# Kernel tuning notes

Measured on AMD Instinct MI355X. Metric: run time of the kernel, lower is better.

The kernel has to match this reference:

```python
import jax, jax.numpy as jnp
import numpy as np

B, N, HID, NH = 8, 1024, 1024, 16
HD = HID // NH  # head_dim = 64
MLP = 4 * HID
EPS = 1e-6


def _xavier(key, fan_in, fan_out):
    lim = np.sqrt(6.0 / (fan_in + fan_out))
    return jax.random.uniform(key, (fan_in, fan_out), jnp.float32, -lim, lim)


def setup_inputs() -> dict:
    key = jax.random.key(0)
    ks = jax.random.split(key, 10)
    return {
        "x": jax.random.normal(ks[0], (B, N, HID), jnp.float32),
        "c": jax.random.normal(ks[1], (B, HID), jnp.float32),
        "w_ada": _xavier(ks[2], HID, 6 * HID), "b_ada": jnp.zeros((6 * HID,), jnp.float32),
        "wq": _xavier(ks[3], HID, HID), "bq": jnp.zeros((HID,), jnp.float32),
        "wk": _xavier(ks[4], HID, HID), "bk": jnp.zeros((HID,), jnp.float32),
        "wv": _xavier(ks[5], HID, HID), "bv": jnp.zeros((HID,), jnp.float32),
        "wo": _xavier(ks[6], HID, HID), "bo": jnp.zeros((HID,), jnp.float32),
        "w1": _xavier(ks[7], HID, MLP), "b1": jnp.zeros((MLP,), jnp.float32),
        "w2": _xavier(ks[8], MLP, HID), "b2": jnp.zeros((HID,), jnp.float32),
    }


def _ln(t):
    # LayerNorm, elementwise_affine=False, eps=1e-6
    mu = jnp.mean(t, axis=-1, keepdims=True)
    var = jnp.mean(jnp.square(t - mu), axis=-1, keepdims=True)
    return (t - mu) * jax.lax.rsqrt(var + EPS)


def _modulate(t, shift, scale):
    return t * (1.0 + scale[:, None, :]) + shift[:, None, :]


def reference(x, c, w_ada, b_ada, wq, bq, wk, bk, wv, bv, wo, bo, w1, b1, w2, b2):
    cmod = jax.nn.silu(c) @ w_ada + b_ada  # [B, 6*HID]
    sh_msa, sc_msa, g_msa, sh_mlp, sc_mlp, g_mlp = jnp.split(cmod, 6, axis=-1)

    xm = _modulate(_ln(x), sh_msa, sc_msa)  # [B, N, HID]
    q = (xm @ wq + bq).reshape(B, N, NH, HD)
    k = (xm @ wk + bk).reshape(B, N, NH, HD)
    v = (xm @ wv + bv).reshape(B, N, NH, HD)

    # NOTE: original scales by 1/head_dim (not 1/sqrt(head_dim)), fp32 softmax
    scores = jnp.einsum('bihd,bjhd->bhij', q, k) / HD
    attn = jax.nn.softmax(scores.astype(jnp.float32), axis=-1)
    out = jnp.einsum('bhij,bjhd->bihd', attn, v).astype(v.dtype)
    out = out.reshape(B, N, HID) @ wo + bo

    x = x + g_msa[:, None, :] * out

    xm2 = _modulate(_ln(x), sh_mlp, sc_mlp)
    h = jax.nn.gelu(xm2 @ w1 + b1, approximate=False)  # nn.GELU default = exact
    mlp_out = h @ w2 + b2
    return x + g_mlp[:, None, :] * mlp_out
```

## Files before the change

### kernel.cpp

```cpp
#include <hip/hip_runtime.h>
#include <hip/hip_bf16.h>
#include <cstdint>


typedef __bf16 bf16;
typedef __attribute__((ext_vector_type(8))) __bf16 bf16x8;
typedef __attribute__((ext_vector_type(4))) __bf16 bf16x4;
typedef __attribute__((ext_vector_type(4))) float f32x4;

#define SEQ   1024
#define NHID  1024
#define NHEAD 16
#define HDIM  64
#define CMS   6144

#define GLD16(gp, lp)                                                  \
  __builtin_amdgcn_global_load_lds(                                    \
      (const __attribute__((address_space(1))) void*)(gp),             \
      (__attribute__((address_space(3))) void*)(lp), 16, 0, 0)

template <int N> __device__ __forceinline__ void vmwait() {
  if constexpr (N == 0)      asm volatile("s_waitcnt vmcnt(0)" ::: "memory");
  else if constexpr (N == 5) asm volatile("s_waitcnt vmcnt(5)" ::: "memory");
  else if constexpr (N == 6) asm volatile("s_waitcnt vmcnt(6)" ::: "memory");
}

#define BAR()                                                          \
  { asm volatile("" ::: "memory");                                     \
    __builtin_amdgcn_s_barrier();                                      \
    asm volatile("" ::: "memory"); }

struct TP4 { const float* s[4]; bf16* d[4]; };

__global__ __launch_bounds__(256) void transpose_conv4(TP4 p)
{
  __shared__ float tile[32][33];
  const float* __restrict__ src = p.s[blockIdx.z];
  bf16* __restrict__ dst = p.d[blockIdx.z];
  int n0 = blockIdx.x * 32, k0 = blockIdx.y * 32;
  int tx = threadIdx.x & 31, ty = threadIdx.x >> 5;
#pragma unroll
  for (int i = 0; i < 32; i += 8)
    tile[ty + i][tx] = src[(size_t)(k0 + ty + i) * 1024 + n0 + tx];
  __syncthreads();
#pragma unroll
  for (int i = 0; i < 32; i += 8)
    dst[(size_t)(n0 + ty + i) * 1024 + k0 + tx] = (bf16)tile[tx][ty + i];
}

__global__ __launch_bounds__(256) void transpose_conv(
    const float* __restrict__ src, bf16* __restrict__ dst, int K, int N)
{
  __shared__ float tile[32][33];
  int n0 = blockIdx.x * 32, k0 = blockIdx.y * 32;
  int tx = threadIdx.x & 31, ty = threadIdx.x >> 5;
#pragma unroll
  for (int i = 0; i < 32; i += 8)
    tile[ty + i][tx] = src[(size_t)(k0 + ty + i) * N + n0 + tx];
  __syncthreads();
#pragma unroll
  for (int i = 0; i < 32; i += 8)
    dst[(size_t)(n0 + ty + i) * K + k0 + tx] = (bf16)tile[tx][ty + i];
}

__global__ __launch_bounds__(256) void ada_kernel(
    const float* __restrict__ c, const float* __restrict__ w_ada,
    const float* __restrict__ b_ada, float* __restrict__ cmod)
{
  __shared__ float cs[1024];
  int b = blockIdx.y;
  int col = blockIdx.x * 256 + threadIdx.x;
  for (int i = threadIdx.x; i < 1024; i += 256) {
    float cv = c[b * 1024 + i];
    cs[i] = cv / (1.0f + __expf(-cv));
  }
  __syncthreads();
  float acc = b_ada[col];
#pragma unroll 8
  for (int kk = 0; kk < 1024; kk++)
    acc += cs[kk] * w_ada[(size_t)kk * CMS + col];
  cmod[b * CMS + col] = acc;
}

__global__ __launch_bounds__(256) void ln_mod(
    const float* __restrict__ x, const float* __restrict__ cmod,
    bf16* __restrict__ out, int sh_off, int sc_off)
{
  int row = blockIdx.x, b = row >> 10, tid = threadIdx.x;
  const float4* xr = (const float4*)(x + (size_t)row * NHID);
  float4 v = xr[tid];
  float s  = v.x + v.y + v.z + v.w;
  float s2 = v.x * v.x + v.y * v.y + v.z * v.z + v.w * v.w;
#pragma unroll
  for (int off = 32; off; off >>= 1) {
    s  += __shfl_xor(s, off);
    s2 += __shfl_xor(s2, off);
  }
  __shared__ float red1[4], red2[4];
  int wave = tid >> 6, lane = tid & 63;
  if (lane == 0) { red1[wave] = s; red2[wave] = s2; }
  __syncthreads();
  float S  = red1[0] + red1[1] + red1[2] + red1[3];
  float S2 = red2[0] + red2[1] + red2[2] + red2[3];
  float mean = S * (1.0f / NHID);
  float var  = S2 * (1.0f / NHID) - mean * mean;
  float rs   = rsqrtf(var + 1e-6f);
  const float4* shp = (const float4*)(cmod + b * CMS + sh_off);
  const float4* scp = (const float4*)(cmod + b * CMS + sc_off);
  float4 sh4 = shp[tid], sc4 = scp[tid];
  bf16x4 o4;
  o4[0] = (bf16)((v.x - mean) * rs * (1.0f + sc4.x) + sh4.x);
  o4[1] = (bf16)((v.y - mean) * rs * (1.0f + sc4.y) + sh4.y);
  o4[2] = (bf16)((v.z - mean) * rs * (1.0f + sc4.z) + sh4.z);
  o4[3] = (bf16)((v.w - mean) * rs * (1.0f + sc4.w) + sh4.w);
  *(bf16x4*)(out + (size_t)row * NHID + tid * 4) = o4;
}

template <int EPI, int BN>
__global__ __launch_bounds__(512, 2) void gemm8(
    const bf16* __restrict__ A, const bf16* __restrict__ Bt,
    const float* __restrict__ bias, const float* __restrict__ bias2,
    const float* __restrict__ bias3,
    bf16* __restrict__ outb, bf16* __restrict__ outb2,
    bf16* __restrict__ outb3, float* __restrict__ outf,
    const float* __restrict__ cmod, int gate_off,
    const float* __restrict__ resid,
    int N, int K)
{
  constexpr int BNH   = BN / 2;
  constexpr int LB    = BNH / 64;
  constexpr int MF    = BN / 64;
  constexpr int WC    = BN / 64;
  constexpr int WRS   = MF * 16;
  constexpr int VMN   = (LB == 2) ? 6 : 5;
  constexpr int BOFF  = 65536;
  constexpr int BBUF  = BNH * 256;
  constexpr int BHALF = BNH * 128;

  extern __shared__ __align__(16) char smem[];

  const int tid  = threadIdx.x;
  const int bm = blockIdx.y * 256, bn = blockIdx.x * BN;
  const int wave = tid >> 6, lane = tid & 63;
  const int wr = wave / WC, wc = wave % WC;
  const int l16 = lane & 15, q4 = lane >> 4;

  const int rq = tid >> 3;
  const int ch = ((tid & 7) ^ (rq & 7)) * 8;
  const int wbase = (tid & 448) * 16;

  const int aRowB = (wr * WRS + l16) * 128;
  const int bRowB = (wc * 32 + l16) * 128;
  const int slotB = (q4 ^ (l16 & 7)) * 16;

  f32x4 acc[2][2][MF][2];
#pragma unroll
  for (int a0 = 0; a0 < 2; a0++)
#pragma unroll
    for (int a1 = 0; a1 < 2; a1++)
#pragma unroll
      for (int a2 = 0; a2 < MF; a2++)
#pragma unroll
        for (int a3 = 0; a3 < 2; a3++) acc[a0][a1][a2][a3] = (f32x4)0.0f;

  auto stA = [&](int buf, int half, int T) {
    const bf16* g = A + (size_t)(bm + half * 128 + rq) * K + T * 64 + ch;
    char* l = smem + buf * 32768 + half * 16384 + wbase;
    GLD16(g, l);
    GLD16(g + (size_t)64 * K, l + 8192);
  };
  auto stB = [&](int buf, int half, int T) {
    const bf16* g = Bt + (size_t)(bn + half * BNH + rq) * K + T * 64 + ch;
    char* l = smem + BOFF + buf * BBUF + half * BHALF + wbase;
    GLD16(g, l);
    if constexpr (LB == 2) { GLD16(g + (size_t)64 * K, l + 8192); }
  };

#define RDA(BUF, QM, FR)                                                   \
  { const char* ab_ = smem + (BUF) * 32768 + (QM) * 16384 + aRowB;         \
    _Pragma("unroll")                                                      \
    for (int ks = 0; ks < 2; ks++) {                                       \
      const int sb_ = slotB ^ (ks * 64);                                   \
      _Pragma("unroll")                                                    \
      for (int mf = 0; mf < MF; mf++)                                      \
        FR[ks][mf] = *(const bf16x8*)(ab_ + mf * 2048 + sb_);              \
    } }

#define RDB(BUF, QN, FR)                                                   \
  { const char* bb_ = smem + BOFF + (BUF) * BBUF + (QN) * BHALF + bRowB;   \
    _Pragma("unroll")                                                      \
    for (int ks = 0; ks < 2; ks++) {                                       \
      const int sb_ = slotB ^ (ks * 64);                                   \
      _Pragma("unroll")                                                    \
      for (int nf = 0; nf < 2; nf++)                                       \
        FR[ks][nf] = *(const bf16x8*)(bb_ + nf * 2048 + sb_);              \
    } }

#define MM(QM, QN, AF, BF)                                                 \
  { __builtin_amdgcn_s_setprio(1);                                         \
    _Pragma("unroll")                                                      \
    for (int mf = 0; mf < MF; mf++)                                        \
      _Pragma("unroll")                                                    \
      for (int nf = 0; nf < 2; nf++) {                                     \
        acc[QM][QN][mf][nf] = __builtin_amdgcn_mfma_f32_16x16x32_bf16(     \
            AF[0][mf], BF[0][nf], acc[QM][QN][mf][nf], 0, 0, 0);           \
        acc[QM][QN][mf][nf] = __builtin_amdgcn_mfma_f32_16x16x32_bf16(     \
            AF[1][mf], BF[1][nf], acc[QM][QN][mf][nf], 0, 0, 0);           \
      }                                                                    \
    __builtin_amdgcn_s_setprio(0); }

  const int NT = K >> 6, NI = NT >> 1;

  bf16x8 afr[2][MF], bfr0[2][2], bfr1[2][2];

  stA(0, 0, 0); stB(0, 0, 0); stB(0, 1, 0); stA(0, 1, 0);
  stA(1, 0, 1); stB(1, 0, 1); stB(1, 1, 1); stA(1, 1, 1);

  for (int i = 0; i < NI; ++i) {
    const int t = 2 * i;
    const int u2 = (t + 2 < NT) ? t + 2 : 0;
    const int u3 = (t + 3 < NT) ? t + 3 : 0;
    vmwait<VMN>(); BAR();
    RDA(0, 0, afr); RDB(0, 0, bfr0);
    MM(0, 0, afr, bfr0);
    BAR();
    RDB(0, 1, bfr1);
    stA(0, 0, u2); stB(0, 0, u2);
    MM(0, 1, afr, bfr1);
    BAR();
    RDA(0, 1, afr);
    stB(0, 1, u2);
    MM(1, 1, afr, bfr1);
    BAR();
    stA(0, 1, u2);
    MM(1, 0, afr, bfr0);
    vmwait<VMN>(); BAR();
    RDA(1, 0, afr); RDB(1, 0, bfr0);
    MM(0, 0, afr, bfr0);
    BAR();
    RDB(1, 1, bfr1);
    stA(1, 0, u3); stB(1, 0, u3);
    MM(0, 1, afr, bfr1);
    BAR();
    RDA(1, 1, afr);
    stB(1, 1, u3);
    MM(1, 1, afr, bfr1);
    BAR();
    stA(1, 1, u3);
    MM(1, 0, afr, bfr0);
  }
  vmwait<0>();
#undef RDA
#undef RDB
#undef MM

  const int colBase = bn + wc * 32 + l16;
  const int rowBase = bm + wr * WRS + q4 * 4;
#pragma unroll
  for (int qm = 0; qm < 2; qm++)
#pragma unroll
  for (int qn = 0; qn < 2; qn++)
#pragma unroll
  for (int mf = 0; mf < MF; mf++)
#pragma unroll
  for (int nf = 0; nf < 2; nf++) {
    const int col  = colBase + qn * BNH + nf * 16;
    const int row0 = rowBase + qm * 128 + mf * 16;
    f32x4 v = acc[qm][qn][mf][nf];
    if constexpr (EPI == 5) {
      const int sel = bn >> 10;
      const float* bp = (sel == 0) ? bias : (sel == 1) ? bias2 : bias3;
      const int colq = col & 1023;
      const float bcol = bp[colq];
      if (sel == 2) {
        bf16x4 o4;
#pragma unroll
        for (int r = 0; r < 4; r++) o4[r] = (bf16)(v[r] + bcol);
        const int bidx = row0 >> 10;
        *(bf16x4*)(outb3 + ((size_t)bidx * NHID + colq) * SEQ +
                   (row0 & 1023)) = o4;
      } else {
        bf16* qk = (sel == 0) ? outb : outb2;
#pragma unroll
        for (int r = 0; r < 4; r++)
          qk[(size_t)(row0 + r) * 1024 + colq] = (bf16)(v[r] + bcol);
      }
    } else if constexpr (EPI == 2) {
      const float bcol = bias[col];
#pragma unroll
      for (int r = 0; r < 4; r++) {
        float val = v[r] + bcol;
        float u2g = 2.0f * val * (0.7978845608f + 0.0356774081f * val * val);
        float e = __expf(u2g);
        float th = 1.0f - 2.0f / (e + 1.0f);
        outb[(size_t)(row0 + r) * N + col] = (bf16)(0.5f * val * (1.0f + th));
      }
    } else {
      const float bcol = bias[col];
#pragma unroll
      for (int r = 0; r < 4; r++) {
        const int row = row0 + r;
        const float gg = cmod[(row >> 10) * CMS + gate_off + col];
        outf[(size_t)row * N + col] =
            resid[(size_t)row * N + col] + gg * (v[r] + bcol);
      }
    }
  }
}

__global__ __launch_bounds__(256) void attn_mfma(
    const bf16* __restrict__ q, const bf16* __restrict__ k,
    const bf16* __restrict__ vt, bf16* __restrict__ o)
{
  __shared__ __align__(16) bf16 Ks[64 * 64];
  __shared__ __align__(16) bf16 Vs[64 * 64];
  __shared__ __align__(16) bf16 Ps[4][32 * 72];

  int bid = blockIdx.x;
  int qt = bid & 7, h = (bid >> 3) & 15, b = bid >> 7;
  int tid = threadIdx.x, wave = tid >> 6, lane = tid & 63;
  int quad = lane >> 4, l16 = lane & 15;
  int qbase = qt * 128 + wave * 32;

  bf16x8 qf[2][2];
  const bf16* qp = q + ((size_t)(b * SEQ + qbase)) * NHID + h * HDIM;
#pragma unroll
  for (int nt = 0; nt < 2; nt++)
#pragma unroll
    for (int kk = 0; kk < 2; kk++) {
      bf16x8 t = *(const bf16x8*)(qp + (size_t)(nt * 16 + l16) * NHID +
                                  kk * 32 + quad * 8);
#pragma unroll
      for (int j = 0; j < 8; j++) t[j] = (bf16)((float)t[j] * 0.015625f);
      qf[nt][kk] = t;
    }

  f32x4 oacc[4][2];
#pragma unroll
  for (int mt = 0; mt < 4; mt++)
#pragma unroll
    for (int nt = 0; nt < 2; nt++) oacc[mt][nt] = (f32x4)0.0f;
  float m_[2] = {-3.0e38f, -3.0e38f}, l_[2] = {0.0f, 0.0f};

  const bf16* kb = k + ((size_t)(b * SEQ)) * NHID + h * HDIM;
  const bf16* vb = vt + ((size_t)(b * NHID + h * HDIM)) * SEQ;

  const int sr0 = tid >> 3, sc0 = tid & 7;

  for (int kt = 0; kt < 16; kt++) {
    __syncthreads();
#pragma unroll
    for (int i = 0; i < 2; i++) {
      int r = i * 32 + sr0;
      int cg = (sc0 ^ (r & 7)) * 8;
      bf16* lk = Ks + (size_t)(i * 256 + (tid & 192)) * 8;
      bf16* lv = Vs + (size_t)(i * 256 + (tid & 192)) * 8;
      GLD16(kb + (size_t)(kt * 64 + r) * NHID + cg, lk);
      GLD16(vb + (size_t)r * SEQ + kt * 64 + cg, lv);
    }
    __syncthreads();

    f32x4 sacc[4][2];
#pragma unroll
    for (int mt = 0; mt < 4; mt++)
#pragma unroll
      for (int nt = 0; nt < 2; nt++) sacc[mt][nt] = (f32x4)0.0f;
#pragma unroll
    for (int kk = 0; kk < 2; kk++) {
      bf16x8 kf[4];
#pragma unroll
      for (int mt = 0; mt < 4; mt++) {
        int row = mt * 16 + l16;
        kf[mt] = *(const bf16x8*)(Ks + row * 64 +
                                  (((kk * 4 + quad) ^ (row & 7)) * 8));
      }
#pragma unroll
      for (int mt = 0; mt < 4; mt++)
#pragma unroll
        for (int nt = 0; nt < 2; nt++)
          sacc[mt][nt] = __builtin_amdgcn_mfma_f32_16x16x32_bf16(
              kf[mt], qf[nt][kk], sacc[mt][nt], 0, 0, 0);
    }

    float alpha[2];
#pragma unroll
    for (int nt = 0; nt < 2; nt++) {
      float tm = -3.0e38f;
#pragma unroll
      for (int mt = 0; mt < 4; mt++)
#pragma unroll
        for (int r = 0; r < 4; r++) tm = fmaxf(tm, sacc[mt][nt][r]);
      tm = fmaxf(tm, __shfl_xor(tm, 16));
      tm = fmaxf(tm, __shfl_xor(tm, 32));
      float mn = fmaxf(m_[nt], tm);
      alpha[nt] = __expf(m_[nt] - mn);
      m_[nt] = mn;
      float ts = 0.0f;
#pragma unroll
      for (int mt = 0; mt < 4; mt++) {
        bf16x4 pv;
#pragma unroll
        for (int r = 0; r < 4; r++) {
          float p = __expf(sacc[mt][nt][r] - mn);
          ts += p;
          pv[r] = (bf16)p;
        }
        *(bf16x4*)(&Ps[wave][(nt * 16 + l16) * 72 + mt * 16 + quad * 4]) = pv;
      }
      ts += __shfl_xor(ts, 16);
      ts += __shfl_xor(ts, 32);
      l_[nt] = l_[nt] * alpha[nt] + ts;
    }
#pragma unroll
    for (int mt = 0; mt < 4; mt++)
#pragma unroll
      for (int nt = 0; nt < 2; nt++)
#pragma unroll
        for (int r = 0; r < 4; r++) oacc[mt][nt][r] *= alpha[nt];

    __asm__ volatile("s_waitcnt lgkmcnt(0)" ::: "memory");

#pragma unroll
    for (int kk = 0; kk < 2; kk++) {
      bf16x8 vf[4], pf[2];
#pragma unroll
      for (int mt = 0; mt < 4; mt++) {
        int row = mt * 16 + l16;
        vf[mt] = *(const bf16x8*)(Vs + row * 64 +
                                  (((kk * 4 + quad) ^ (row & 7)) * 8));
      }
#pragma unroll
      for (int nt = 0; nt < 2; nt++)
        pf[nt] = *(const bf16x8*)(&Ps[wave][(nt * 16 + l16) * 72 +
                                            kk * 32 + quad * 8]);
#pragma unroll
      for (int mt = 0; mt < 4; mt++)
#pragma unroll
        for (int nt = 0; nt < 2; nt++)
          oacc[mt][nt] = __builtin_amdgcn_mfma_f32_16x16x32_bf16(
              vf[mt], pf[nt], oacc[mt][nt], 0, 0, 0);
    }
  }

#pragma unroll
  for (int nt = 0; nt < 2; nt++) {
    float rl = 1.0f / l_[nt];
#pragma unroll
    for (int mt = 0; mt < 4; mt++) {
      bf16x4 o4;
#pragma unroll
      for (int r = 0; r < 4; r++) o4[r] = (bf16)(oacc[mt][nt][r] * rl);
      *(bf16x4*)(o + ((size_t)(b * SEQ + qbase + nt * 16 + l16)) * NHID +
                 h * HDIM + mt * 16 + quad * 4) = o4;
    }
  }
}

#define OFF_CMOD 0u
#define OFF_WQT  196608u
#define OFF_WKT  (OFF_WQT + 2097152u)
#define OFF_WVT  (OFF_WKT + 2097152u)
#define OFF_WOT  (OFF_WVT + 2097152u)
#define OFF_W1T  (OFF_WOT + 2097152u)
#define OFF_W2T  (OFF_W1T + 8388608u)
#define OFF_X2   (OFF_W2T + 8388608u)
#define OFF_XM2  (OFF_X2  + 33554432u)
#define OFF_POOL (OFF_XM2 + 16777216u)

extern "C" void kernel_launch(void* const* d_in, const int* in_sizes, int n_in,
                              void* d_out, int out_size, void* d_ws, size_t ws_size,
                              hipStream_t stream)
{
  const float* x     = (const float*)d_in[0];
  const float* c     = (const float*)d_in[1];
  const float* w_ada = (const float*)d_in[2];
  const float* b_ada = (const float*)d_in[3];
  const float* wq = (const float*)d_in[4];  const float* bq = (const float*)d_in[5];
  const float* wk = (const float*)d_in[6];  const float* bk = (const float*)d_in[7];
  const float* wv = (const float*)d_in[8];  const float* bv = (const float*)d_in[9];
  const float* wo = (const float*)d_in[10]; const float* bo = (const float*)d_in[11];
  const float* w1 = (const float*)d_in[12]; const float* b1 = (const float*)d_in[13];
  const float* w2 = (const float*)d_in[14]; const float* b2 = (const float*)d_in[15];
  float* out = (float*)d_out;
  char* ws = (char*)d_ws;

  float* cmod = (float*)(ws + OFF_CMOD);
  bf16* wqT = (bf16*)(ws + OFF_WQT);
  bf16* wkT = (bf16*)(ws + OFF_WKT);
  bf16* wvT = (bf16*)(ws + OFF_WVT);
  bf16* woT = (bf16*)(ws + OFF_WOT);
  bf16* w1T = (bf16*)(ws + OFF_W1T);
  bf16* w2T = (bf16*)(ws + OFF_W2T);
  float* x2 = (float*)(ws + OFF_X2);
  bf16* xm2 = (bf16*)(ws + OFF_XM2);
  bf16* xm  = (bf16*)(ws + OFF_POOL);
  bf16* qb  = (bf16*)(ws + OFF_POOL + 16777216u);
  bf16* kb  = (bf16*)(ws + OFF_POOL + 33554432u);
  bf16* vtb = (bf16*)(ws + OFF_POOL + 50331648u);
  bf16* ob  = xm;
  bf16* hb  = xm;

  static bool attr_set = false;
  if (!attr_set) {
    hipFuncSetAttribute(reinterpret_cast<const void*>(&gemm8<5, 128>),
                        hipFuncAttributeMaxDynamicSharedMemorySize, 98304);
    hipFuncSetAttribute(reinterpret_cast<const void*>(&gemm8<1, 128>),
                        hipFuncAttributeMaxDynamicSharedMemorySize, 98304);
    hipFuncSetAttribute(reinterpret_cast<const void*>(&gemm8<2, 256>),
                        hipFuncAttributeMaxDynamicSharedMemorySize, 131072);
    hipFuncSetAttribute(reinterpret_cast<const void*>(&gemm8<3, 128>),
                        hipFuncAttributeMaxDynamicSharedMemorySize, 98304);
    attr_set = true;
  }

  TP4 tp;
  tp.s[0] = wq; tp.s[1] = wk; tp.s[2] = wv; tp.s[3] = wo;
  tp.d[0] = wqT; tp.d[1] = wkT; tp.d[2] = wvT; tp.d[3] = woT;
  transpose_conv4<<<dim3(32, 32, 4), 256, 0, stream>>>(tp);
  transpose_conv<<<dim3(128, 32), 256, 0, stream>>>(w1, w1T, 1024, 4096);
  transpose_conv<<<dim3(32, 128), 256, 0, stream>>>(w2, w2T, 4096, 1024);

  ada_kernel<<<dim3(24, 8), 256, 0, stream>>>(c, w_ada, b_ada, cmod);

  ln_mod<<<8192, 256, 0, stream>>>(x, cmod, xm, 0, 1024);

  gemm8<5, 128><<<dim3(24, 32), 512, 98304, stream>>>(
      xm, wqT, bq, bk, bv, qb, kb, vtb, nullptr, nullptr, 0, nullptr,
      1024, 1024);

  attn_mfma<<<1024, 256, 0, stream>>>(qb, kb, vtb, ob);

  gemm8<1, 128><<<dim3(8, 32), 512, 98304, stream>>>(
      ob, woT, bo, nullptr, nullptr, nullptr, nullptr, nullptr, x2,
      cmod, 2048, x, 1024, 1024);

  ln_mod<<<8192, 256, 0, stream>>>(x2, cmod, xm2, 3072, 4096);

  gemm8<2, 256><<<dim3(16, 32), 512, 131072, stream>>>(
      xm2, w1T, b1, nullptr, nullptr, hb, nullptr, nullptr, nullptr,
      nullptr, 0, nullptr, 4096, 1024);

  gemm8<3, 128><<<dim3(8, 32), 512, 98304, stream>>>(
      hb, w2T, b2, nullptr, nullptr, nullptr, nullptr, nullptr, out,
      cmod, 5120, x2, 1024, 4096);
}
```

Baseline: 579.3 us.

## Restructure GEMM main loop with finer-grained barriers and staggered global-to-LDS loads

```diff
diff --git a/kernel.cpp b/kernel.cpp
--- a/kernel.cpp
+++ b/kernel.cpp
@@ -21,7 +21,7 @@
 
 template <int N> __device__ __forceinline__ void vmwait() {
   if constexpr (N == 0)      asm volatile("s_waitcnt vmcnt(0)" ::: "memory");
-  else if constexpr (N == 5) asm volatile("s_waitcnt vmcnt(5)" ::: "memory");
+  else if constexpr (N == 4) asm volatile("s_waitcnt vmcnt(4)" ::: "memory");
   else if constexpr (N == 6) asm volatile("s_waitcnt vmcnt(6)" ::: "memory");
 }
 
@@ -29,6 +29,8 @@
   { asm volatile("" ::: "memory");                                     \
     __builtin_amdgcn_s_barrier();                                      \
     asm volatile("" ::: "memory"); }
+
+#define LGKM0() asm volatile("s_waitcnt lgkmcnt(0)" ::: "memory")
 
 struct TP4 { const float* s[4]; bf16* d[4]; };
 
@@ -131,8 +133,8 @@
   constexpr int LB    = BNH / 64;
   constexpr int MF    = BN / 64;
   constexpr int WC    = BN / 64;
-  constexpr int WRS   = MF * 16;
-  constexpr int VMN   = (LB == 2) ? 6 : 5;
+  constexpr int WRS   = 256 / (8 / WC) / 2;
+  constexpr int VMN   = (LB == 2) ? 6 : 4;
   constexpr int BOFF  = 65536;
   constexpr int BBUF  = BNH * 256;
   constexpr int BHALF = BNH * 128;
@@ -214,40 +216,54 @@
   bf16x8 afr[2][MF], bfr0[2][2], bfr1[2][2];
 
   stA(0, 0, 0); stB(0, 0, 0); stB(0, 1, 0); stA(0, 1, 0);
-  stA(1, 0, 1); stB(1, 0, 1); stB(1, 1, 1); stA(1, 1, 1);
+  stA(1, 0, 1); stB(1, 0, 1); stB(1, 1, 1);
+  vmwait<VMN>();
+  BAR();
 
   for (int i = 0; i < NI; ++i) {
     const int t = 2 * i;
-    const int u2 = (t + 2 < NT) ? t + 2 : 0;
-    const int u3 = (t + 3 < NT) ? t + 3 : 0;
-    vmwait<VMN>(); BAR();
+    const int u2 = (t + 2 < NT) ? t + 2 : NT - 2;
+    const int u3 = (t + 3 < NT) ? t + 3 : NT - 1;
     RDA(0, 0, afr); RDB(0, 0, bfr0);
+    stA(1, 1, t + 1);
+    BAR(); LGKM0();
     MM(0, 0, afr, bfr0);
     BAR();
     RDB(0, 1, bfr1);
-    stA(0, 0, u2); stB(0, 0, u2);
+    stA(0, 0, u2);
+    BAR(); LGKM0();
     MM(0, 1, afr, bfr1);
     BAR();
     RDA(0, 1, afr);
+    stB(0, 0, u2);
+    BAR(); LGKM0();
+    MM(1, 1, afr, bfr1);
+    BAR();
     stB(0, 1, u2);
+    vmwait<VMN>();
+    BAR();
+    MM(1, 0, afr, bfr0);
+    BAR();
+    RDA(1, 0, afr); RDB(1, 0, bfr0);
+    stA(0, 1, u2);
+    BAR(); LGKM0();
+    MM(0, 0, afr, bfr0);
+    BAR();
+    RDB(1, 1, bfr1);
+    stA(1, 0, u3);
+    BAR(); LGKM0();
+    MM(0, 1, afr, bfr1);
+    BAR();
+    RDA(1, 1, afr);
+    stB(1, 0, u3);
+    BAR(); LGKM0();
     MM(1, 1, afr, bfr1);
     BAR();
-    stA(0, 1, u2);
+    stB(1, 1, u3);
+    vmwait<VMN>();
+    BAR();
     MM(1, 0, afr, bfr0);
-    vmwait<VMN>(); BAR();
-    RDA(1, 0, afr); RDB(1, 0, bfr0);
-    MM(0, 0, afr, bfr0);
-    BAR();
-    RDB(1, 1, bfr1);
-    stA(1, 0, u3); stB(1, 0, u3);
-    MM(0, 1, afr, bfr1);
-    BAR();
-    RDA(1, 1, afr);
-    stB(1, 1, u3);
-    MM(1, 1, afr, bfr1);
-    BAR();
-    stA(1, 1, u3);
-    MM(1, 0, afr, bfr0);
+    BAR();
   }
   vmwait<0>();
 #undef RDA
```

Result: slower. 604.3 us (+4.3%).
